# Performance work log

Measured on AMD Instinct MI355X. Metric: run time of the kernel, lower is better.

Reference implementation:

```python
import jax, jax.numpy as jnp
import numpy as np

# quantization formats
E_Q, M_Q = 4, 3      # E4M3 fp8 for input/param quantizers
E_A, M_A = 5, 10     # fp16-like accumulate / output format


def quant(x, exp, man):
    """Round-to-nearest-even float quantization to (exp, man) bits,
    with subnormals and saturation (mptorch float_quantize semantics)."""
    ebias = 2 ** (exp - 1) - 1
    emin = 1 - ebias                      # min normal exponent
    maxv = (2.0 - 2.0 ** (-man)) * 2.0 ** ebias
    ax = jnp.abs(x)
    e = jnp.floor(jnp.log2(jnp.where(ax > 0, ax, 1.0)))
    e = jnp.maximum(e, emin)              # subnormal range shares emin scale
    scale = jnp.exp2(man - e)
    q = jnp.round(x * scale) / scale      # jnp.round is half-to-even
    return jnp.clip(q, -maxv, maxv)


def qgemm(x, wt, exp_add, man_add):
    """Custom-precision GEMM x[M,K] @ wt[K,N] with fma=True:
    the running accumulator is requantized to (exp_add, man_add)
    after every rank-1 (per-k) fused multiply-add."""
    M, K = x.shape
    N = wt.shape[1]

    def step(acc, xw):
        xk, wk = xw                       # [M], [N]
        acc = quant(acc + xk[:, None] * wk[None, :], exp_add, man_add)
        return acc, None

    acc0 = jnp.zeros((M, N), x.dtype)
    acc, _ = jax.lax.scan(step, acc0, (x.T, wt))
    return acc


def setup_inputs() -> dict:
    key = jax.random.key(0)
    k1, k2, k3 = jax.random.split(key, 3)
    in_f, out_f, m = 1024, 1024, 2048
    x = jax.random.normal(k1, (m, in_f), jnp.float32)
    weight = jax.random.normal(k2, (out_f, in_f), jnp.float32) / np.float32(np.sqrt(in_f))
    bound = 1.0 / np.float32(np.sqrt(in_f))
    bias = jax.random.uniform(k3, (out_f,), jnp.float32, -bound, bound)
    return {"x": x, "weight": weight, "bias": bias}


def reference(x, weight, bias):
    qx = quant(x, E_Q, M_Q)               # input_quant
    qw = quant(weight, E_Q, M_Q)          # param_quant
    qb = quant(bias, E_Q, M_Q)            # param_quant
    out = qgemm(qx, qw.T, E_A, M_A)       # float_gemm with fma accumulation
    out = out + qb[None, :]
    out = quant(out, E_A, M_A)            # output requantization
    return out
```

## Files before the change

### kernel.cpp

```cpp
#include <hip/hip_runtime.h>
#include <hip/hip_fp16.h>


#define M_DIM 2048
#define N_DIM 1024
#define K_DIM 1024

#define BM 32
#define BN 128
#define BK 64
#define NCHUNK (K_DIM / BK)

typedef unsigned u32;
typedef float f32x2 __attribute__((ext_vector_type(2)));
typedef _Float16 f16x2 __attribute__((ext_vector_type(2)));

__device__ __forceinline__ float quant_e4m3(float v) {
  unsigned au = __float_as_uint(v) & 0x7fffffffu;
  if (au == 0u) return v;
  int e = (int)(au >> 23) - 127;
  if (e < -6) e = -6;
  float s  = __uint_as_float((unsigned)(130 - e) << 23);
  float is = __uint_as_float((unsigned)(124 + e) << 23);
  float r = rintf(v * s) * is;
  return fminf(240.f, fmaxf(-240.f, r));
}

__device__ __forceinline__ u32 enc_e4m3(float v) {
  unsigned au = __float_as_uint(v);
  unsigned sg = (au >> 24) & 0x80u;
  unsigned a = au & 0x7fffffffu;
  if (a == 0u) return sg;
  int e = (int)(a >> 23) - 127;
  unsigned man = (a >> 20) & 7u;
  if (e >= -6) return sg | ((unsigned)(e + 7) << 3) | man;
  return sg | ((8u | man) >> (-6 - e));
}

__global__ __launch_bounds__(256) void prep_kernel(const float* __restrict__ x,
                                                   const float* __restrict__ w,
                                                   u32* __restrict__ xP,
                                                   u32* __restrict__ wB) {
  __shared__ float tile[32][33];
  const int tx = threadIdx.x & 31;
  const int ty = threadIdx.x >> 5;
  if (blockIdx.x < 2048) {
    const int c0 = (blockIdx.x & 31) * 32;
    const int r0 = (blockIdx.x >> 5) * 32;
#pragma unroll
    for (int i = 0; i < 4; i++) {
      int r = r0 + ty + i * 8;
      tile[ty + i * 8][tx] = quant_e4m3(x[(size_t)r * K_DIM + c0 + tx]);
    }
    __syncthreads();
#pragma unroll
    for (int i = 0; i < 2; i++) {
      int tl = ty + i * 8;
      u32 lo = (u32)__half_as_ushort(__float2half(tile[tx][2 * tl]));
      u32 hi = (u32)__half_as_ushort(__float2half(tile[tx][2 * tl + 1]));
      xP[(size_t)(c0 / 2 + tl) * M_DIM + r0 + tx] = lo | (hi << 16);
    }
  } else {
    const int b = blockIdx.x - 2048;
    const int k0t = (b & 31) * 32;
    const int n0t = (b >> 5) * 32;
#pragma unroll
    for (int i = 0; i < 4; i++) {
      int n = n0t + ty + i * 8;
      tile[ty + i * 8][tx] = quant_e4m3(w[(size_t)n * K_DIM + k0t + tx]);
    }
    __syncthreads();
    const int u = threadIdx.x & 3;
    const int cl = (threadIdx.x >> 2) & 7;
    const int ql = (threadIdx.x >> 5) & 7;
    const int nl = 4 * cl + 2 * (u & 1);
    const int kl = 4 * ql + 2 * (u >> 1);
    u32 v = enc_e4m3(tile[nl][kl])
          | (enc_e4m3(tile[nl + 1][kl]) << 8)
          | (enc_e4m3(tile[nl][kl + 1]) << 16)
          | (enc_e4m3(tile[nl + 1][kl + 1]) << 24);
    wB[(size_t)(k0t / 4 + ql) * N_DIM + n0t + (cl << 2) + u] = v;
  }
}


__device__ __forceinline__ void gld16(const void* g, void* l) {
  __builtin_amdgcn_global_load_lds((const __attribute__((address_space(1))) u32*)g,
                                   (__attribute__((address_space(3))) u32*)l, 16, 0, 0);
}

#if __has_builtin(__builtin_amdgcn_cvt_scalef32_pk_f16_fp8)
template <int HI>
__device__ __forceinline__ u32 fp8x2_h2(u32 v) {
  f16x2 h = __builtin_amdgcn_cvt_scalef32_pk_f16_fp8((int)v, 1.0f, HI != 0);
  return __builtin_bit_cast(u32, h);
}
#else
template <int HI>
__device__ __forceinline__ u32 fp8x2_h2(u32 v) {
  f32x2 f = __builtin_amdgcn_cvt_pk_f32_fp8((int)v, HI);
  u32 r;
  asm("v_cvt_pkrtz_f16_f32 %0, %1, %2" : "=v"(r) : "v"(f[0]), "v"(f[1]));
  return r;
}
#endif

__device__ __forceinline__ void pkfma_lo(u32& acc, u32 x, u32 w) {
  asm("v_pk_fma_f16 %0, %1, %2, %0 op_sel:[0,0,0] op_sel_hi:[0,1,1]"
      : "+v"(acc) : "v"(x), "v"(w));
}
__device__ __forceinline__ void pkfma_hi(u32& acc, u32 x, u32 w) {
  asm("v_pk_fma_f16 %0, %1, %2, %0 op_sel:[1,0,0] op_sel_hi:[1,1,1]"
      : "+v"(acc) : "v"(x), "v"(w));
}

__global__ __launch_bounds__(256, 2) void gemm_qfma(const u32* __restrict__ xP,
                                                    const u32* __restrict__ wB,
                                                    const float* __restrict__ b,
                                                    float* __restrict__ outp) {
  __shared__ __align__(16) u32 xs[2][BK / 2][BM];
  __shared__ __align__(16) u32 wsu[2][BK / 4][BN];
  const int tid = threadIdx.x;
  const int tn = tid & 31;
  const int tm = tid >> 5;
  const int bn0 = blockIdx.x * BN;
  const int bm0 = blockIdx.y * BM;

  u32 acc[4][2];
#pragma unroll
  for (int i = 0; i < 4; i++) { acc[i][0] = 0u; acc[i][1] = 0u; }

  const u32* xsrc = xP + (size_t)(tid >> 3) * M_DIM + bm0 + ((tid & 7) << 2);
  const u32* wsrc = wB + (size_t)(tid >> 5) * N_DIM + bn0 + ((tid & 31) << 2);

  auto stage = [&](int ch, int buf) {
    gld16(xsrc + (size_t)ch * (BK / 2) * M_DIM, (char*)&xs[buf][0][0] + tid * 16);
    const u32* wp = wsrc + (size_t)ch * (BK / 4) * N_DIM;
    char* wl = (char*)&wsu[buf][0][0] + tid * 16;
    gld16(wp, wl);
    gld16(wp + (size_t)8 * N_DIM, wl + 4096);
  };

  auto compute = [&](int buf) {
#pragma unroll
    for (int q = 0; q < BK / 4; q++) {
      const uint4 xv  = *reinterpret_cast<const uint4*>(&xs[buf][2 * q][tm << 2]);
      const uint4 xv2 = *reinterpret_cast<const uint4*>(&xs[buf][2 * q + 1][tm << 2]);
      const uint4 wq  = *reinterpret_cast<const uint4*>(&wsu[buf][q][tn << 2]);
      const u32 wk0a = fp8x2_h2<0>(wq.x);
      const u32 wk1a = fp8x2_h2<1>(wq.x);
      const u32 wk0b = fp8x2_h2<0>(wq.y);
      const u32 wk1b = fp8x2_h2<1>(wq.y);
      const u32 wk2a = fp8x2_h2<0>(wq.z);
      const u32 wk3a = fp8x2_h2<1>(wq.z);
      const u32 wk2b = fp8x2_h2<0>(wq.w);
      const u32 wk3b = fp8x2_h2<1>(wq.w);
      pkfma_lo(acc[0][0], xv.x, wk0a); pkfma_lo(acc[0][1], xv.x, wk0b);
      pkfma_lo(acc[1][0], xv.y, wk0a); pkfma_lo(acc[1][1], xv.y, wk0b);
      pkfma_lo(acc[2][0], xv.z, wk0a); pkfma_lo(acc[2][1], xv.z, wk0b);
      pkfma_lo(acc[3][0], xv.w, wk0a); pkfma_lo(acc[3][1], xv.w, wk0b);
      pkfma_hi(acc[0][0], xv.x, wk1a); pkfma_hi(acc[0][1], xv.x, wk1b);
      pkfma_hi(acc[1][0], xv.y, wk1a); pkfma_hi(acc[1][1], xv.y, wk1b);
      pkfma_hi(acc[2][0], xv.z, wk1a); pkfma_hi(acc[2][1], xv.z, wk1b);
      pkfma_hi(acc[3][0], xv.w, wk1a); pkfma_hi(acc[3][1], xv.w, wk1b);
      pkfma_lo(acc[0][0], xv2.x, wk2a); pkfma_lo(acc[0][1], xv2.x, wk2b);
      pkfma_lo(acc[1][0], xv2.y, wk2a); pkfma_lo(acc[1][1], xv2.y, wk2b);
      pkfma_lo(acc[2][0], xv2.z, wk2a); pkfma_lo(acc[2][1], xv2.z, wk2b);
      pkfma_lo(acc[3][0], xv2.w, wk2a); pkfma_lo(acc[3][1], xv2.w, wk2b);
      pkfma_hi(acc[0][0], xv2.x, wk3a); pkfma_hi(acc[0][1], xv2.x, wk3b);
      pkfma_hi(acc[1][0], xv2.y, wk3a); pkfma_hi(acc[1][1], xv2.y, wk3b);
      pkfma_hi(acc[2][0], xv2.z, wk3a); pkfma_hi(acc[2][1], xv2.z, wk3b);
      pkfma_hi(acc[3][0], xv2.w, wk3a); pkfma_hi(acc[3][1], xv2.w, wk3b);
    }
  };

  stage(0, 0);
  __syncthreads();
#pragma unroll 1
  for (int ch = 0; ch < NCHUNK; ch += 2) {
    stage(ch + 1, 1);
    compute(0);
    __syncthreads();
    if (ch + 2 < NCHUNK) stage(ch + 2, 0);
    compute(1);
    __syncthreads();
  }

  const int nc = bn0 + (tn << 2);
  float4 bq;
  bq.x = quant_e4m3(b[nc + 0]);
  bq.y = quant_e4m3(b[nc + 1]);
  bq.z = quant_e4m3(b[nc + 2]);
  bq.w = quant_e4m3(b[nc + 3]);
#pragma unroll
  for (int i = 0; i < 4; i++) {
    __half2 a0 = *reinterpret_cast<__half2*>(&acc[i][0]);
    __half2 a1 = *reinterpret_cast<__half2*>(&acc[i][1]);
    float4 o;
    o.x = __half2float(__float2half(__low2float(a0)  + bq.x));
    o.y = __half2float(__float2half(__high2float(a0) + bq.y));
    o.z = __half2float(__float2half(__low2float(a1)  + bq.z));
    o.w = __half2float(__float2half(__high2float(a1) + bq.w));
    *reinterpret_cast<float4*>(
        outp + (size_t)(bm0 + (tm << 2) + i) * N_DIM + nc) = o;
  }
}

extern "C" void kernel_launch(void* const* d_in, const int* in_sizes, int n_in,
                              void* d_out, int out_size, void* d_ws, size_t ws_size,
                              hipStream_t stream) {
  const float* x = (const float*)d_in[0];
  const float* w = (const float*)d_in[1];
  const float* b = (const float*)d_in[2];
  float* outp = (float*)d_out;

  char* ws_ = (char*)d_ws;
  u32* xP = (u32*)ws_;
  u32* wB = (u32*)(ws_ + (size_t)(4 << 20));

  hipLaunchKernelGGL(prep_kernel, dim3(2048 + 1024), dim3(256), 0, stream,
                     x, w, xP, wB);
  hipLaunchKernelGGL(gemm_qfma, dim3(N_DIM / BN, M_DIM / BM), dim3(256), 0, stream,
                     xP, wB, b, outp);
}
```

Baseline: 119.7 us.

## Use single-wave 32x32 GEMM blocks and replace barriers with waitcnt drains

The GEMM moves from 256-thread blocks computing 32x128 tiles to 64-thread, single-wavefront blocks computing 32x32 tiles, giving four times as many blocks. Because each block is one wave, the __syncthreads barriers are replaced by an s_waitcnt vmcnt(0)/lgkmcnt(0) drain plus a scheduling barrier. The main loop becomes a simple per-chunk double-buffer rotation. The goal is to remove block-wide barrier stalls and give the scheduler more independent waves. The cost is less operand reuse per block, so x and w tiles are re-read from L2 more often.

```diff
diff --git a/kernel.cpp b/kernel.cpp
--- a/kernel.cpp
+++ b/kernel.cpp
@@ -6,8 +6,7 @@
 #define N_DIM 1024
 #define K_DIM 1024
 
-#define BM 32
-#define BN 128
+#define BT 32
 #define BK 64
 #define NCHUNK (K_DIM / BK)
 
@@ -114,31 +113,63 @@
       : "+v"(acc) : "v"(x), "v"(w));
 }
 
-__global__ __launch_bounds__(256, 2) void gemm_qfma(const u32* __restrict__ xP,
-                                                    const u32* __restrict__ wB,
-                                                    const float* __restrict__ b,
-                                                    float* __restrict__ outp) {
-  __shared__ __align__(16) u32 xs[2][BK / 2][BM];
-  __shared__ __align__(16) u32 wsu[2][BK / 4][BN];
-  const int tid = threadIdx.x;
-  const int tn = tid & 31;
-  const int tm = tid >> 5;
-  const int bn0 = blockIdx.x * BN;
-  const int bm0 = blockIdx.y * BM;
+__global__ __launch_bounds__(64, 2) void gemm_qfma(const u32* __restrict__ xP,
+                                                   const u32* __restrict__ wB,
+                                                   const float* __restrict__ b,
+                                                   float* __restrict__ outp) {
+  __shared__ __align__(16) u32 xs[2][BK / 2][BT];
+  __shared__ __align__(16) u32 wsu[2][BK / 4][BT];
+  const int l = threadIdx.x;
+  const int tn = l & 7;
+  const int tm = l >> 3;
+  const int bn0 = blockIdx.x * BT;
+  const int bm0 = blockIdx.y * BT;
 
   u32 acc[4][2];
 #pragma unroll
   for (int i = 0; i < 4; i++) { acc[i][0] = 0u; acc[i][1] = 0u; }
 
-  const u32* xsrc = xP + (size_t)(tid >> 3) * M_DIM + bm0 + ((tid & 7) << 2);
-  const u32* wsrc = wB + (size_t)(tid >> 5) * N_DIM + bn0 + ((tid & 31) << 2);
+  const u32* xsrc = xP + (size_t)(l >> 3) * M_DIM + bm0 + ((l & 7) << 2);
+  const u32* wsrc = wB + (size_t)(l >> 3) * N_DIM + bn0 + ((l & 7) << 2);
 
   auto stage = [&](int ch, int buf) {
-    gld16(xsrc + (size_t)ch * (BK / 2) * M_DIM, (char*)&xs[buf][0][0] + tid * 16);
+    const u32* xp = xsrc + (size_t)ch * (BK / 2) * M_DIM;
+    char* xl = (char*)&xs[buf][0][0] + l * 16;
+#pragma unroll
+    for (int p = 0; p < 4; p++)
+      gld16(xp + (size_t)(p * 8) * M_DIM, xl + p * 1024);
     const u32* wp = wsrc + (size_t)ch * (BK / 4) * N_DIM;
-    char* wl = (char*)&wsu[buf][0][0] + tid * 16;
-    gld16(wp, wl);
-    gld16(wp + (size_t)8 * N_DIM, wl + 4096);
+    char* wl = (char*)&wsu[buf][0][0] + l * 16;
+#pragma unroll
+    for (int p = 0; p < 2; p++)
+      gld16(wp + (size_t)(p * 8) * N_DIM, wl + p * 1024);
+  };
+
+  auto quad = [&](const uint4& xv, const uint4& xv2, const uint4& wq) {
+    const u32 wk0a = fp8x2_h2<0>(wq.x);
+    const u32 wk1a = fp8x2_h2<1>(wq.x);
+    const u32 wk0b = fp8x2_h2<0>(wq.y);
+    const u32 wk1b = fp8x2_h2<1>(wq.y);
+    const u32 wk2a = fp8x2_h2<0>(wq.z);
+    const u32 wk3a = fp8x2_h2<1>(wq.z);
+    const u32 wk2b = fp8x2_h2<0>(wq.w);
+    const u32 wk3b = fp8x2_h2<1>(wq.w);
+    pkfma_lo(acc[0][0], xv.x, wk0a); pkfma_lo(acc[0][1], xv.x, wk0b);
+    pkfma_lo(acc[1][0], xv.y, wk0a); pkfma_lo(acc[1][1], xv.y, wk0b);
+    pkfma_lo(acc[2][0], xv.z, wk0a); pkfma_lo(acc[2][1], xv.z, wk0b);
+    pkfma_lo(acc[3][0], xv.w, wk0a); pkfma_lo(acc[3][1], xv.w, wk0b);
+    pkfma_hi(acc[0][0], xv.x, wk1a); pkfma_hi(acc[0][1], xv.x, wk1b);
+    pkfma_hi(acc[1][0], xv.y, wk1a); pkfma_hi(acc[1][1], xv.y, wk1b);
+    pkfma_hi(acc[2][0], xv.z, wk1a); pkfma_hi(acc[2][1], xv.z, wk1b);
+    pkfma_hi(acc[3][0], xv.w, wk1a); pkfma_hi(acc[3][1], xv.w, wk1b);
+    pkfma_lo(acc[0][0], xv2.x, wk2a); pkfma_lo(acc[0][1], xv2.x, wk2b);
+    pkfma_lo(acc[1][0], xv2.y, wk2a); pkfma_lo(acc[1][1], xv2.y, wk2b);
+    pkfma_lo(acc[2][0], xv2.z, wk2a); pkfma_lo(acc[2][1], xv2.z, wk2b);
+    pkfma_lo(acc[3][0], xv2.w, wk2a); pkfma_lo(acc[3][1], xv2.w, wk2b);
+    pkfma_hi(acc[0][0], xv2.x, wk3a); pkfma_hi(acc[0][1], xv2.x, wk3b);
+    pkfma_hi(acc[1][0], xv2.y, wk3a); pkfma_hi(acc[1][1], xv2.y, wk3b);
+    pkfma_hi(acc[2][0], xv2.z, wk3a); pkfma_hi(acc[2][1], xv2.z, wk3b);
+    pkfma_hi(acc[3][0], xv2.w, wk3a); pkfma_hi(acc[3][1], xv2.w, wk3b);
   };
 
   auto compute = [&](int buf) {
@@ -147,43 +178,22 @@
       const uint4 xv  = *reinterpret_cast<const uint4*>(&xs[buf][2 * q][tm << 2]);
       const uint4 xv2 = *reinterpret_cast<const uint4*>(&xs[buf][2 * q + 1][tm << 2]);
       const uint4 wq  = *reinterpret_cast<const uint4*>(&wsu[buf][q][tn << 2]);
-      const u32 wk0a = fp8x2_h2<0>(wq.x);
-      const u32 wk1a = fp8x2_h2<1>(wq.x);
-      const u32 wk0b = fp8x2_h2<0>(wq.y);
-      const u32 wk1b = fp8x2_h2<1>(wq.y);
-      const u32 wk2a = fp8x2_h2<0>(wq.z);
-      const u32 wk3a = fp8x2_h2<1>(wq.z);
-      const u32 wk2b = fp8x2_h2<0>(wq.w);
-      const u32 wk3b = fp8x2_h2<1>(wq.w);
-      pkfma_lo(acc[0][0], xv.x, wk0a); pkfma_lo(acc[0][1], xv.x, wk0b);
-      pkfma_lo(acc[1][0], xv.y, wk0a); pkfma_lo(acc[1][1], xv.y, wk0b);
-      pkfma_lo(acc[2][0], xv.z, wk0a); pkfma_lo(acc[2][1], xv.z, wk0b);
-      pkfma_lo(acc[3][0], xv.w, wk0a); pkfma_lo(acc[3][1], xv.w, wk0b);
-      pkfma_hi(acc[0][0], xv.x, wk1a); pkfma_hi(acc[0][1], xv.x, wk1b);
-      pkfma_hi(acc[1][0], xv.y, wk1a); pkfma_hi(acc[1][1], xv.y, wk1b);
-      pkfma_hi(acc[2][0], xv.z, wk1a); pkfma_hi(acc[2][1], xv.z, wk1b);
-      pkfma_hi(acc[3][0], xv.w, wk1a); pkfma_hi(acc[3][1], xv.w, wk1b);
-      pkfma_lo(acc[0][0], xv2.x, wk2a); pkfma_lo(acc[0][1], xv2.x, wk2b);
-      pkfma_lo(acc[1][0], xv2.y, wk2a); pkfma_lo(acc[1][1], xv2.y, wk2b);
-      pkfma_lo(acc[2][0], xv2.z, wk2a); pkfma_lo(acc[2][1], xv2.z, wk2b);
-      pkfma_lo(acc[3][0], xv2.w, wk2a); pkfma_lo(acc[3][1], xv2.w, wk2b);
-      pkfma_hi(acc[0][0], xv2.x, wk3a); pkfma_hi(acc[0][1], xv2.x, wk3b);
-      pkfma_hi(acc[1][0], xv2.y, wk3a); pkfma_hi(acc[1][1], xv2.y, wk3b);
-      pkfma_hi(acc[2][0], xv2.z, wk3a); pkfma_hi(acc[2][1], xv2.z, wk3b);
-      pkfma_hi(acc[3][0], xv2.w, wk3a); pkfma_hi(acc[3][1], xv2.w, wk3b);
-    }
+      quad(xv, xv2, wq);
+    }
+  };
+
+  auto drain = [&]() {
+    asm volatile("s_waitcnt vmcnt(0) lgkmcnt(0)" ::: "memory");
+    __builtin_amdgcn_sched_barrier(0);
   };
 
   stage(0, 0);
-  __syncthreads();
+  drain();
 #pragma unroll 1
-  for (int ch = 0; ch < NCHUNK; ch += 2) {
-    stage(ch + 1, 1);
-    compute(0);
-    __syncthreads();
-    if (ch + 2 < NCHUNK) stage(ch + 2, 0);
-    compute(1);
-    __syncthreads();
+  for (int ch = 0; ch < NCHUNK; ch++) {
+    if (ch + 1 < NCHUNK) stage(ch + 1, (ch + 1) & 1);
+    compute(ch & 1);
+    drain();
   }
 
   const int nc = bn0 + (tn << 2);
@@ -220,6 +230,6 @@
 
   hipLaunchKernelGGL(prep_kernel, dim3(2048 + 1024), dim3(256), 0, stream,
                      x, w, xP, wB);
-  hipLaunchKernelGGL(gemm_qfma, dim3(N_DIM / BN, M_DIM / BM), dim3(256), 0, stream,
+  hipLaunchKernelGGL(gemm_qfma, dim3(N_DIM / BT, M_DIM / BT), dim3(64), 0, stream,
                      xP, wB, b, outp);
 }
```

Measured after the change: 137.8 us. +15.1%, slower.
